# Kernel tuning notes

Measured on AMD Instinct MI355X. Metric: run time of the kernel, lower is better.

Reference implementation:

```python
import jax, jax.numpy as jnp
import numpy as np

B, C, E, HLR, WLR = 2, 64, 4, 192, 192


def setup_inputs() -> dict:
    key = jax.random.key(0)
    ks = jax.random.split(key, 8)
    s = 0.05  # keep activations/offsets in a sane range
    return {
        "x": jax.random.normal(ks[0], (B, C, HLR, WLR), jnp.float32),
        "fused": jax.random.normal(ks[1], (B, C, HLR, WLR), jnp.float32),
        "weight_compress": jax.random.normal(ks[2], (E, C // 8, C), jnp.float32) * s,
        "weight_expand": jax.random.normal(ks[3], (E, C, C // 8), jnp.float32) * s,
        "body_w1": jax.random.normal(ks[4], (64, 4), jnp.float32) * s,
        "body_b1": jnp.zeros((64,), jnp.float32),
        "body_w2": jax.random.normal(ks[5], (64, 64), jnp.float32) * s,
        "body_b2": jnp.zeros((64,), jnp.float32),
        "routing_w": jax.random.normal(ks[6], (E, 64), jnp.float32) * s,
        "routing_b": jnp.zeros((E,), jnp.float32),
        "offset_w": jax.random.normal(ks[7], (2, 64), jnp.float32) * s,
        "offset_b": jnp.zeros((2,), jnp.float32),
        "scale": 2,
    }


def _conv1x1(x, w, b):
    # x: [n, cin, H, W], w: [cout, cin] (1x1 conv)
    return jnp.einsum('oc,nchw->nohw', w, x) + b[None, :, None, None]


def _grid_sample(img, px, py):
    # Bilinear sample, align_corners=True semantics, zeros padding.
    # img: [b,c,h,w]; px, py: [b,H,W] absolute LR pixel coords.
    b, c, h, w = img.shape
    x0 = jnp.floor(px)
    y0 = jnp.floor(py)
    wx = (px - x0)[:, None]  # [b,1,H,W]
    wy = (py - y0)[:, None]

    def gather(xi, yi):
        valid = (xi >= 0) & (xi <= w - 1) & (yi >= 0) & (yi <= h - 1)
        xc = jnp.clip(xi, 0, w - 1).astype(jnp.int32)
        yc = jnp.clip(yi, 0, h - 1).astype(jnp.int32)
        v = jax.vmap(lambda im, yy, xx: im[:, yy, xx])(img, yc, xc)  # [b,c,H,W]
        return v * valid[:, None].astype(img.dtype)

    v00 = gather(x0, y0)
    v01 = gather(x0 + 1, y0)
    v10 = gather(x0, y0 + 1)
    v11 = gather(x0 + 1, y0 + 1)
    top = v00 * (1 - wx) + v01 * wx
    bot = v10 * (1 - wx) + v11 * wx
    return top * (1 - wy) + bot * wy


def reference(x, fused, weight_compress, weight_expand, body_w1, body_b1,
              body_w2, body_b2, routing_w, routing_b, offset_w, offset_b, scale):
    b, c, h, w = fused.shape
    H, W = round(h * scale), round(w * scale)
    e, c8 = weight_compress.shape[0], weight_compress.shape[1]

    ch = jnp.arange(H, dtype=jnp.float32)
    cw = jnp.arange(W, dtype=jnp.float32)
    coor_h = (ch + 0.5) / scale - jnp.floor((ch + 0.5) / scale + 0.001) - 0.5  # [H]
    coor_w = (cw + 0.5) / scale - jnp.floor((cw + 0.5) / scale + 0.001) - 0.5  # [W]
    inp = jnp.stack([
        jnp.full((H, W), 1.0 / scale, jnp.float32),
        jnp.full((H, W), 1.0 / scale, jnp.float32),
        jnp.broadcast_to(coor_h[:, None], (H, W)),
        jnp.broadcast_to(coor_w[None, :], (H, W)),
    ], 0)[None]  # [1,4,H,W]

    emb = jax.nn.relu(_conv1x1(inp, body_w1, body_b1))
    emb = jax.nn.relu(_conv1x1(emb, body_w2, body_b2))
    offset = _conv1x1(emb, offset_w, offset_b)            # [1,2,H,W]
    routing = jax.nn.sigmoid(_conv1x1(emb, routing_w, routing_b))  # [1,E,H,W]

    rw = routing.reshape(e, H * W).T                      # [HW, E]
    wc = (rw @ weight_compress.reshape(e, -1)).reshape(H, W, c8, c)  # per-pixel compress
    we = (rw @ weight_expand.reshape(e, -1)).reshape(H, W, c, c8)    # per-pixel expand

    # deformable sample: HR grid projected into LR space + learned offset (pixel units)
    px = jnp.broadcast_to((cw[None, :] + 0.5) / scale - 0.5, (H, W))[None] + offset[:, 0]
    py = jnp.broadcast_to((ch[:, None] + 0.5) / scale - 0.5, (H, W))[None] + offset[:, 1]
    px = jnp.broadcast_to(px, (b, H, W))
    py = jnp.broadcast_to(py, (b, H, W))
    fea0 = _grid_sample(fused, px, py)                    # [b,c,H,W]

    fea = fea0.transpose(0, 2, 3, 1)                      # [b,H,W,c]
    mid = jnp.einsum('hwoc,bhwc->bhwo', wc, fea)          # [b,H,W,c//8]
    out = jnp.einsum('hwco,bhwo->bhwc', we, mid)          # [b,H,W,c]
    return out.transpose(0, 3, 1, 2) + fea0
```

## Files before the change

kernel.cpp:

```cpp
#include <hip/hip_runtime.h>
#include <hip/hip_fp16.h>
#include <math.h>

typedef __attribute__((ext_vector_type(8))) _Float16 half8;
typedef __attribute__((ext_vector_type(4))) float f32x4;

#define HLR_ 192
#define WLR_ 192
#define H_ 384
#define W_ 384
#define LRP (HLR_*WLR_)
#define TPX 96
#define NTW (W_/TPX)
#define IPW 48
#define NCOL 52
#define XBMAX (WLR_-NCOL)

#define WS_OFF_OFF 8192

__device__ __forceinline__ unsigned short f32_f16(float x){
    union { _Float16 h; unsigned short u; } c; c.h = (_Float16)x; return c.u;
}
__device__ __forceinline__ unsigned int pk_f16(float a, float b){
    union { _Float16 h[2]; unsigned int u; } c;
    c.h[0] = (_Float16)a; c.h[1] = (_Float16)b; return c.u;
}
__device__ __forceinline__ half8 splat8h(_Float16 h){
    half8 v = {h,h,h,h,h,h,h,h};
    return v;
}

__global__ __launch_bounds__(256) void prep_kernel(
    const float* __restrict__ w1, const float* __restrict__ b1,
    const float* __restrict__ w2, const float* __restrict__ b2,
    const float* __restrict__ rw, const float* __restrict__ rb,
    const float* __restrict__ ow, const float* __restrict__ ob,
    const float* __restrict__ WC, const float* __restrict__ WE,
    unsigned short* __restrict__ Kmat, float* __restrict__ g_off)
{
    __shared__ float smem[8912];
    int tid = threadIdx.x;

    float* sW2 = smem;
    float* sRW = smem + 4160;
    float* sE1 = smem + 4544;
    float* sR  = smem + 4800;
    float* sWc = smem + 4816;
    float* sWe = smem + 6864;

    for (int idx = tid; idx < 4096; idx += 256)
        sW2[(idx>>6)*65 + (idx&63)] = w2[idx];
    sRW[tid] = rw[tid];
    if (tid < 128) sRW[256 + tid] = ow[tid];

    int wave = tid >> 6, lane = tid & 63;
    int ph = wave >> 1, pw = wave & 1;

    float ch = (ph + 0.5f)*0.5f;
    float coor_h = ch - floorf(ch + 0.001f) - 0.5f;
    float cw = (pw + 0.5f)*0.5f;
    float coor_w = cw - floorf(cw + 0.001f) - 0.5f;

    float e1 = w1[lane*4+0]*0.5f + w1[lane*4+1]*0.5f
             + w1[lane*4+2]*coor_h + w1[lane*4+3]*coor_w + b1[lane];
    sE1[wave*64 + lane] = fmaxf(e1, 0.0f);
    __syncthreads();

    float e2 = b2[lane];
    #pragma unroll 16
    for (int i = 0; i < 64; ++i) e2 += sW2[lane*65 + i] * sE1[wave*64 + i];
    e2 = fmaxf(e2, 0.0f);

    #pragma unroll
    for (int k = 0; k < 6; ++k) {
        float t = sRW[k*64 + lane] * e2;
        #pragma unroll
        for (int m = 1; m <= 32; m <<= 1) t += __shfl_xor(t, m, 64);
        if (lane == 0) {
            if (k < 4) sR[wave*4 + k] = 1.0f/(1.0f + expf(-(t + rb[k])));
            else       g_off[wave*2 + (k-4)] = t + ob[k-4];
        }
    }
    __syncthreads();

    for (int idx = tid; idx < 2048; idx += 256) {
        int cls = idx >> 9, rem = idx & 511;
        float r0=sR[cls*4+0], r1=sR[cls*4+1], r2=sR[cls*4+2], r3=sR[cls*4+3];
        sWc[cls*512 + rem] =
            r0*WC[0*512+rem] + r1*WC[1*512+rem] + r2*WC[2*512+rem] + r3*WC[3*512+rem];
    }
    for (int idx = tid; idx < 2048; idx += 256) {
        int cls = idx >> 9, rem = idx & 511;
        float r0=sR[cls*4+0], r1=sR[cls*4+1], r2=sR[cls*4+2], r3=sR[cls*4+3];
        sWe[cls*512 + rem] =
            r0*WE[0*512+rem] + r1*WE[1*512+rem] + r2*WE[2*512+rem] + r3*WE[3*512+rem];
    }
    __syncthreads();

    for (int idx = tid; idx < 16384; idx += 256) {
        int cls = idx >> 12, rem = idx & 4095;
        int c = rem >> 6, cp = rem & 63;
        float a = (c == cp) ? 1.0f : 0.0f;
        #pragma unroll
        for (int o = 0; o < 8; ++o)
            a += sWe[cls*512 + c*8 + o] * sWc[cls*512 + o*64 + cp];
        Kmat[idx] = f32_f16(a);
    }
}

__global__ __launch_bounds__(256, 5) void main_kernel(
    const float* __restrict__ fused, const unsigned short* __restrict__ Kmat,
    const float* __restrict__ g_off, float* __restrict__ out)
{
    __shared__ __align__(16) unsigned short sFea[4*NCOL*64];

    int g = blockIdx.x;
    int xcd = g & 7;
    int t = g >> 3;
    int q = t >> 2;
    int wt = t & 3;
    int h = xcd*48 + q;
    int w0 = wt * TPX;
    int tid = threadIdx.x, wave = tid >> 6, lane = tid & 63;
    int b = wave >> 1, par = wave & 1;
    int ph = h & 1, cls = ph*2 + par;

    float off0 = g_off[cls*2 + 0];
    float off1 = g_off[cls*2 + 1];

    float py  = (h + 0.5f)*0.5f - 0.5f + off1;
    float y0f = floorf(py);
    float wy  = py - y0f;
    int   y0  = (int)y0f;
    float fy0 = (y0 >= 0  && y0 <= HLR_-1) ? 1.0f : 0.0f;
    float fy1 = (y0 >= -1 && y0 <= HLR_-2) ? 1.0f : 0.0f;
    int   yc0 = min(max(y0, 0), HLR_-1);
    int   yc1 = min(max(y0+1, 0), HLR_-1);
    float A0 = (1.0f - wy)*fy0;
    float A1 = wy*fy1;

    float pxb  = (w0 + par + 0.5f)*0.5f - 0.5f + off0;
    float x0bf = floorf(pxb);
    float wx   = pxb - x0bf;
    int   x0b  = (int)x0bf;
    float omwx = 1.0f - wx;

    int xbase4 = min(max(x0b, 0) & ~3, XBMAX);
    int dx = x0b - xbase4;

    unsigned short* rw_base = sFea + wave*(NCOL*64);

    int xg   = lane >> 5;
    int cp   = lane & 31;
    int c0   = cp*2;
    int colb = xg*24;

    const float* base0 = fused + ((size_t)(b*64 + c0)*HLR_ + yc0)*WLR_ + xbase4 + colb;
    const float* base1 = fused + ((size_t)(b*64 + c0)*HLR_ + yc1)*WLR_ + xbase4 + colb;

    f32x4 e[7], f[7];
    {
        f32x4 r0v[7], r1v[7];
        #pragma unroll
        for (int v = 0; v < 7; ++v) r0v[v] = *(const f32x4*)(base0 + 4*v);
        #pragma unroll
        for (int v = 0; v < 7; ++v) r1v[v] = *(const f32x4*)(base1 + 4*v);
        #pragma unroll
        for (int v = 0; v < 7; ++v) e[v] = r0v[v]*A0 + r1v[v]*A1;
    }
    {
        const float* q0p = base0 + LRP;
        const float* q1p = base1 + LRP;
        f32x4 r0v[7], r1v[7];
        #pragma unroll
        for (int v = 0; v < 7; ++v) r0v[v] = *(const f32x4*)(q0p + 4*v);
        #pragma unroll
        for (int v = 0; v < 7; ++v) r1v[v] = *(const f32x4*)(q1p + 4*v);
        #pragma unroll
        for (int v = 0; v < 7; ++v) f[v] = r0v[v]*A0 + r1v[v]*A1;
    }
    int chb = c0 >> 3, coff = c0 & 7;
    #pragma unroll
    for (int v = 0; v < 7; ++v) {
        #pragma unroll
        for (int j = 0; j < 4; ++j) {
            int col = colb + 4*v + j;
            *(unsigned int*)(rw_base + (col<<6) + ((chb ^ (col & 7))<<3) + coff) =
                pk_f16(e[v][j], f[v][j]);
        }
    }
    __syncthreads();

    int lm = lane & 15, lg = lane >> 4;

    const unsigned short* Kc = Kmat + cls*4096;
    half8 Af[4][2];
    #pragma unroll
    for (int mt = 0; mt < 4; ++mt)
        #pragma unroll
        for (int kt = 0; kt < 2; ++kt)
            Af[mt][kt] = *(const half8*)(Kc + (mt*16 + lm)*64 + kt*32 + lg*8);

    #pragma unroll
    for (int nt = 0; nt < 3; ++nt) {
        int slot = nt*16 + lm;
        int x_s = x0b + slot;
        float fxp = (x_s >= 0  && x_s <= WLR_-1) ? 1.0f : 0.0f;
        float fxn = (x_s >= -1 && x_s <= WLR_-2) ? 1.0f : 0.0f;
        int col  = min(max(slot + dx,     0), NCOL-1);
        int col1 = min(max(slot + 1 + dx, 0), NCOL-1);
        _Float16 W0 = (_Float16)(omwx * fxp);
        _Float16 W1 = (_Float16)(wx   * fxn);

        half8 P00 = *(const half8*)(rw_base + (col <<6) + (((0+lg) ^ (col &7))<<3));
        half8 P01 = *(const half8*)(rw_base + (col1<<6) + (((0+lg) ^ (col1&7))<<3));
        half8 P10 = *(const half8*)(rw_base + (col <<6) + (((4+lg) ^ (col &7))<<3));
        half8 P11 = *(const half8*)(rw_base + (col1<<6) + (((4+lg) ^ (col1&7))<<3));
        half8 B0 = P00*splat8h(W0) + P01*splat8h(W1);
        half8 B1 = P10*splat8h(W0) + P11*splat8h(W1);

        int wc = w0 + 2*slot + par;
        #pragma unroll
        for (int mt = 0; mt < 4; ++mt) {
            f32x4 a = {0.0f, 0.0f, 0.0f, 0.0f};
            a = __builtin_amdgcn_mfma_f32_16x16x32_f16(Af[mt][0], B0, a, 0, 0, 0);
            a = __builtin_amdgcn_mfma_f32_16x16x32_f16(Af[mt][1], B1, a, 0, 0, 0);
            int c0r = mt*16 + lg*4;
            float* op = out + (((size_t)(b*64 + c0r)*H_ + h)*W_ + wc);
            op[0*(size_t)(H_*W_)] = a[0];
            op[1*(size_t)(H_*W_)] = a[1];
            op[2*(size_t)(H_*W_)] = a[2];
            op[3*(size_t)(H_*W_)] = a[3];
        }
    }
}

extern "C" void kernel_launch(void* const* d_in, const int* in_sizes, int n_in,
                              void* d_out, int out_size, void* d_ws, size_t ws_size,
                              hipStream_t stream)
{
    const float* fused = (const float*)d_in[1];
    const float* WC    = (const float*)d_in[2];
    const float* WE    = (const float*)d_in[3];
    const float* w1    = (const float*)d_in[4];
    const float* b1    = (const float*)d_in[5];
    const float* w2    = (const float*)d_in[6];
    const float* b2    = (const float*)d_in[7];
    const float* rw    = (const float*)d_in[8];
    const float* rb    = (const float*)d_in[9];
    const float* ow    = (const float*)d_in[10];
    const float* ob    = (const float*)d_in[11];
    (void)in_sizes; (void)n_in; (void)out_size; (void)ws_size;

    float* ws = (float*)d_ws;
    unsigned short* Kmat = (unsigned short*)ws;
    float* g_off = ws + WS_OFF_OFF;
    float* o = (float*)d_out;

    hipLaunchKernelGGL(prep_kernel, dim3(1), dim3(256), 0, stream,
                       w1, b1, w2, b2, rw, rb, ow, ob, WC, WE, Kmat, g_off);
    hipLaunchKernelGGL(main_kernel, dim3(H_*NTW), dim3(256), 0, stream,
                       fused, Kmat, g_off, o);
}
```

Baseline: 160.4 us.

## Restructure LR row staging loads, hash LDS swizzle, hoist K fragment loads

```diff
diff --git a/kernel.cpp b/kernel.cpp
--- a/kernel.cpp
+++ b/kernel.cpp
@@ -29,6 +29,7 @@
     half8 v = {h,h,h,h,h,h,h,h};
     return v;
 }
+__device__ __forceinline__ int chash(int col){ return (col ^ (col >> 2)) & 7; }
 
 __global__ __launch_bounds__(256) void prep_kernel(
     const float* __restrict__ w1, const float* __restrict__ b1,
@@ -108,7 +109,7 @@
     }
 }
 
-__global__ __launch_bounds__(256, 5) void main_kernel(
+__global__ __launch_bounds__(256, 6) void main_kernel(
     const float* __restrict__ fused, const unsigned short* __restrict__ Kmat,
     const float* __restrict__ g_off, float* __restrict__ out)
 {
@@ -128,6 +129,15 @@
     float off0 = g_off[cls*2 + 0];
     float off1 = g_off[cls*2 + 1];
 
+    int lm = lane & 15, lg = lane >> 4;
+    const unsigned short* Kc = Kmat + cls*4096;
+    half8 Af[4][2];
+    #pragma unroll
+    for (int mt = 0; mt < 4; ++mt)
+        #pragma unroll
+        for (int kt = 0; kt < 2; ++kt)
+            Af[mt][kt] = *(const half8*)(Kc + (mt*16 + lm)*64 + kt*32 + lg*8);
+
     float py  = (h + 0.5f)*0.5f - 0.5f + off1;
     float y0f = floorf(py);
     float wy  = py - y0f;
@@ -150,56 +160,31 @@
 
     unsigned short* rw_base = sFea + wave*(NCOL*64);
 
-    int xg   = lane >> 5;
-    int cp   = lane & 31;
-    int c0   = cp*2;
-    int colb = xg*24;
-
-    const float* base0 = fused + ((size_t)(b*64 + c0)*HLR_ + yc0)*WLR_ + xbase4 + colb;
-    const float* base1 = fused + ((size_t)(b*64 + c0)*HLR_ + yc1)*WLR_ + xbase4 + colb;
-
-    f32x4 e[7], f[7];
-    {
-        f32x4 r0v[7], r1v[7];
-        #pragma unroll
-        for (int v = 0; v < 7; ++v) r0v[v] = *(const f32x4*)(base0 + 4*v);
-        #pragma unroll
-        for (int v = 0; v < 7; ++v) r1v[v] = *(const f32x4*)(base1 + 4*v);
-        #pragma unroll
-        for (int v = 0; v < 7; ++v) e[v] = r0v[v]*A0 + r1v[v]*A1;
-    }
-    {
-        const float* q0p = base0 + LRP;
-        const float* q1p = base1 + LRP;
-        f32x4 r0v[7], r1v[7];
-        #pragma unroll
-        for (int v = 0; v < 7; ++v) r0v[v] = *(const f32x4*)(q0p + 4*v);
-        #pragma unroll
-        for (int v = 0; v < 7; ++v) r1v[v] = *(const f32x4*)(q1p + 4*v);
-        #pragma unroll
-        for (int v = 0; v < 7; ++v) f[v] = r0v[v]*A0 + r1v[v]*A1;
-    }
-    int chb = c0 >> 3, coff = c0 & 7;
-    #pragma unroll
-    for (int v = 0; v < 7; ++v) {
-        #pragma unroll
-        for (int j = 0; j < 4; ++j) {
-            int col = colb + 4*v + j;
-            *(unsigned int*)(rw_base + (col<<6) + ((chb ^ (col & 7))<<3) + coff) =
-                pk_f16(e[v][j], f[v][j]);
+    int cp2 = lane / 13;
+    int qx  = lane - cp2*13;
+    if (cp2 < 4) {
+        int xg = xbase4 + 4*qx;
+        const float* p0 = fused + ((size_t)(b*64 + cp2*2)*HLR_ + yc0)*WLR_ + xg;
+        const float* p1 = fused + ((size_t)(b*64 + cp2*2)*HLR_ + yc1)*WLR_ + xg;
+        #pragma unroll
+        for (int it = 0; it < 8; ++it) {
+            const float* a0p = p0 + (size_t)it*8*LRP;
+            const float* a1p = p1 + (size_t)it*8*LRP;
+            f32x4 a0 = *(const f32x4*)(a0p);
+            f32x4 a1 = *(const f32x4*)(a1p);
+            f32x4 b0 = *(const f32x4*)(a0p + LRP);
+            f32x4 b1 = *(const f32x4*)(a1p + LRP);
+            f32x4 e = a0*A0 + a1*A1;
+            f32x4 f = b0*A0 + b1*A1;
+            #pragma unroll
+            for (int j = 0; j < 4; ++j) {
+                int col = 4*qx + j;
+                *(unsigned int*)(rw_base + (col<<6) + ((it ^ chash(col))<<3) + cp2*2) =
+                    pk_f16(e[j], f[j]);
+            }
         }
     }
     __syncthreads();
-
-    int lm = lane & 15, lg = lane >> 4;
-
-    const unsigned short* Kc = Kmat + cls*4096;
-    half8 Af[4][2];
-    #pragma unroll
-    for (int mt = 0; mt < 4; ++mt)
-        #pragma unroll
-        for (int kt = 0; kt < 2; ++kt)
-            Af[mt][kt] = *(const half8*)(Kc + (mt*16 + lm)*64 + kt*32 + lg*8);
 
     #pragma unroll
     for (int nt = 0; nt < 3; ++nt) {
@@ -212,10 +197,10 @@
         _Float16 W0 = (_Float16)(omwx * fxp);
         _Float16 W1 = (_Float16)(wx   * fxn);
 
-        half8 P00 = *(const half8*)(rw_base + (col <<6) + (((0+lg) ^ (col &7))<<3));
-        half8 P01 = *(const half8*)(rw_base + (col1<<6) + (((0+lg) ^ (col1&7))<<3));
-        half8 P10 = *(const half8*)(rw_base + (col <<6) + (((4+lg) ^ (col &7))<<3));
-        half8 P11 = *(const half8*)(rw_base + (col1<<6) + (((4+lg) ^ (col1&7))<<3));
+        half8 P00 = *(const half8*)(rw_base + (col <<6) + (((0+lg) ^ chash(col ))<<3));
+        half8 P01 = *(const half8*)(rw_base + (col1<<6) + (((0+lg) ^ chash(col1))<<3));
+        half8 P10 = *(const half8*)(rw_base + (col <<6) + (((4+lg) ^ chash(col ))<<3));
+        half8 P11 = *(const half8*)(rw_base + (col1<<6) + (((4+lg) ^ chash(col1))<<3));
         half8 B0 = P00*splat8h(W0) + P01*splat8h(W1);
         half8 B1 = P10*splat8h(W0) + P11*splat8h(W1);
 
```

Measured after the change: 150.6 us. -6.1%, faster.
